# Performance work log

Hardware: AMD Instinct MI355X
Metric: run time of the kernel (lower is better)

The kernel has to match this reference:

```python
import jax, jax.numpy as jnp
import numpy as np

D_MODEL = 1024
H = 16
D_K = D_MODEL // H
B, S = 2, 2048

def setup_inputs() -> dict:
    key = jax.random.key(0)
    ks = jax.random.split(key, 13)
    scale = 1.0 / np.sqrt(D_MODEL)
    mk = lambda k: jax.random.normal(k, (D_MODEL, D_MODEL), dtype=jnp.float32) * scale
    return {
        'q': jax.random.normal(ks[0], (B, S, D_MODEL), dtype=jnp.float32),
        'k': jax.random.normal(ks[1], (B, S, D_MODEL), dtype=jnp.float32),
        'v': jax.random.normal(ks[2], (B, S, D_MODEL), dtype=jnp.float32),
        'mask': jax.random.randint(ks[3], (B, 1, S, S), 0, 2, dtype=jnp.int32),
        'wq': mk(ks[4]), 'bq': jnp.zeros((D_MODEL,), jnp.float32),
        'wk': mk(ks[5]), 'bk': jnp.zeros((D_MODEL,), jnp.float32),
        'wv': mk(ks[6]), 'bv': jnp.zeros((D_MODEL,), jnp.float32),
        'wo': mk(ks[7]), 'bo': jnp.zeros((D_MODEL,), jnp.float32),
    }

def reference(q, k, v, mask, wq, bq, wk, bk, wv, bv, wo, bo):
    b, s, _ = q.shape
    # linear projections then split heads: [B,S,D] -> [B,H,S,Dk]
    def proj(x, w, bias):
        y = x @ w + bias
        return y.reshape(b, -1, H, D_K).transpose(0, 2, 1, 3)
    Q = proj(q, wq, bq)
    K = proj(k, wk, bk)
    V = proj(v, wv, bv)
    scores = jnp.einsum('bhqd,bhkd->bhqk', Q, K) / jnp.sqrt(jnp.float32(D_K))
    # faithful to source: masked positions are set to 1e-9 (not -inf)
    scores = jnp.where(mask == 0, jnp.float32(1e-9), scores)
    attn = jax.nn.softmax(scores, axis=-1)  # dropout is identity in eval mode
    x = jnp.einsum('bhqk,bhkd->bhqd', attn, V)
    x = x.transpose(0, 2, 1, 3).reshape(b, s, D_MODEL)
    return x @ wo + bo
```

## Files before the change

### kernel.cpp

```cpp
#include <hip/hip_runtime.h>
#include <hip/hip_bf16.h>

#define DM 1024
#define HEADS 16
#define DKK 64
#define BB 2
#define SS 2048
#define MROWS (BB*SS)

typedef __attribute__((ext_vector_type(8))) short bf16x8;
typedef __attribute__((ext_vector_type(4))) float f32x4;
typedef __attribute__((ext_vector_type(2))) unsigned int uv2;
typedef __hip_bfloat16 bf16;

#define SC2 0.1803368801f
#define MB2 1.442695041e-9f

__device__ __forceinline__ void async16(const void* g, void* l) {
    __builtin_amdgcn_global_load_lds((const __attribute__((address_space(1))) void*)g,
                                     (__attribute__((address_space(3))) void*)l, 16, 0, 0);
}

__global__ void prep_kernel(const float* __restrict__ q, const float* __restrict__ k,
                            const float* __restrict__ v,
                            const float* __restrict__ wq, const float* __restrict__ wk,
                            const float* __restrict__ wv, const float* __restrict__ wo,
                            const int* __restrict__ mask,
                            bf16* __restrict__ qkv, bf16* __restrict__ wcat,
                            unsigned long long* __restrict__ bits) {
    __shared__ float tile[32][33];
    const int bid = blockIdx.x;
    const int tid = threadIdx.x;
    if (bid < 12288) {
        const int z = bid >> 12;
        const int i = ((bid & 4095) << 8) + tid;
        const float* src = z == 0 ? q : (z == 1 ? k : v);
        float4 val = ((const float4*)src)[i];
        union { bf16 b[4]; ushort4 u; } cvt;
        cvt.b[0] = __float2bfloat16(val.x);
        cvt.b[1] = __float2bfloat16(val.y);
        cvt.b[2] = __float2bfloat16(val.z);
        cvt.b[3] = __float2bfloat16(val.w);
        ((ushort4*)(qkv + (size_t)z * MROWS * DM))[i] = cvt.u;
    } else if (bid < 12288 + 4096) {
        const int t = bid - 12288;
        const int z = t >> 10;
        const int bx = t & 31, by = (t >> 5) & 31;
        const float* src = z == 0 ? wq : (z == 1 ? wk : (z == 2 ? wv : wo));
        bf16* dst = wcat + ((size_t)z << 20);
        const int tx = tid & 31, ty = tid >> 5;
        const int x = bx * 32 + tx, y0 = by * 32 + ty;
#pragma unroll
        for (int i = 0; i < 32; i += 8)
            tile[ty + i][tx] = src[(size_t)(y0 + i) * DM + x];
        __syncthreads();
        const int nx = by * 32 + tx, ny0 = bx * 32 + ty;
#pragma unroll
        for (int i = 0; i < 32; i += 8)
            dst[(size_t)(ny0 + i) * DM + nx] = __float2bfloat16(tile[tx][ty + i]);
    } else {
        const int i4 = ((bid - 16384) << 8) + tid;
        const int4 m = ((const int4*)mask)[i4];
        unsigned long long vv = (unsigned long long)(
            (m.x != 0 ? 1u : 0u) | (m.y != 0 ? 2u : 0u) |
            (m.z != 0 ? 4u : 0u) | (m.w != 0 ? 8u : 0u));
        vv <<= ((tid & 15) * 4);
        vv |= __shfl_xor(vv, 1);
        vv |= __shfl_xor(vv, 2);
        vv |= __shfl_xor(vv, 4);
        vv |= __shfl_xor(vv, 8);
        if ((tid & 15) == 0) bits[i4 >> 4] = vv;
    }
}

__global__ __launch_bounds__(256) void gemm_qkv(const bf16* __restrict__ qb, const bf16* __restrict__ kb,
                                                const bf16* __restrict__ vb, const bf16* __restrict__ wcat,
                                                const float* __restrict__ bq, const float* __restrict__ bk,
                                                const float* __restrict__ bv,
                                                bf16* __restrict__ Qh, bf16* __restrict__ Kh,
                                                bf16* __restrict__ Vt) {
    __shared__ __align__(16) bf16 lA[128 * 32];
    __shared__ __align__(16) bf16 lB[128 * 32];
    const int seg = blockIdx.x >> 3;
    const bf16* A    = seg == 0 ? qb : (seg == 1 ? kb : vb);
    const bf16* Bt   = wcat + ((size_t)seg << 20);
    const float* bias = seg == 0 ? bq : (seg == 1 ? bk : bv);

    const int tid  = threadIdx.x;
    const int lane = tid & 63;
    const int lm   = lane & 15;
    const int quad = lane >> 4;
    const int w    = tid >> 6;
    const int wm   = w >> 1, wn = w & 1;
    const int m0   = blockIdx.y * 128;
    const int n0   = (blockIdx.x & 7) * 128;
    const int wbase = w << 6;

    f32x4 acc[4][4];
#pragma unroll
    for (int i = 0; i < 4; ++i)
#pragma unroll
        for (int j = 0; j < 4; ++j) acc[i][j] = (f32x4){0.f, 0.f, 0.f, 0.f};

    for (int kt = 0; kt < DM / 32; ++kt) {
#pragma unroll
        for (int r = 0; r < 2; ++r) {
            const int idx = r * 256 + tid;
            const int row = idx >> 2;
            const int kc  = idx & 3;
            async16(A + (size_t)(m0 + row) * DM + kt * 32 + kc * 8,
                    (char*)lA + (size_t)(r * 256 + wbase) * 16);
            async16(Bt + (size_t)(n0 + row) * DM + kt * 32 + kc * 8,
                    (char*)lB + (size_t)(r * 256 + wbase) * 16);
        }
        __syncthreads();
        bf16x8 af[4], bb[4];
#pragma unroll
        for (int mt = 0; mt < 4; ++mt)
            af[mt] = *(const bf16x8*)&lA[(wm * 64 + mt * 16 + lm) * 32 + quad * 8];
#pragma unroll
        for (int nt = 0; nt < 4; ++nt)
            bb[nt] = *(const bf16x8*)&lB[(wn * 64 + nt * 16 + lm) * 32 + quad * 8];
#pragma unroll
        for (int mt = 0; mt < 4; ++mt)
#pragma unroll
            for (int nt = 0; nt < 4; ++nt)
                acc[mt][nt] = __builtin_amdgcn_mfma_f32_16x16x32_bf16(af[mt], bb[nt], acc[mt][nt], 0, 0, 0);
        __syncthreads();
    }

    if (seg < 2) {
        bf16* outQK = seg == 0 ? Qh : Kh;
        const float oscale = (seg == 1) ? SC2 : 1.0f;
#pragma unroll
        for (int mt = 0; mt < 4; ++mt) {
#pragma unroll
            for (int nt = 0; nt < 4; ++nt) {
                const int gcol = n0 + wn * 64 + nt * 16 + lm;
                const float bvv = bias[gcol];
                const int h = gcol >> 6, d = gcol & 63;
#pragma unroll
                for (int r = 0; r < 4; ++r) {
                    const int grow = m0 + wm * 64 + mt * 16 + quad * 4 + r;
                    const int b = grow >> 11, s = grow & 2047;
                    const float val = (acc[mt][nt][r] + bvv) * oscale;
                    outQK[((size_t)(b * HEADS + h) * SS + s) * DKK + d] = __float2bfloat16(val);
                }
            }
        }
    } else {
#pragma unroll
        for (int mt = 0; mt < 4; ++mt) {
#pragma unroll
            for (int nt = 0; nt < 4; ++nt) {
                const int gcol = n0 + wn * 64 + nt * 16 + lm;
                const float bvv = bias[gcol];
                const int h = gcol >> 6, d = gcol & 63;
                const int growb = m0 + wm * 64 + mt * 16 + quad * 4;
                const int b = growb >> 11, s = growb & 2047;
                union { bf16 hh[4]; uint2 u; } pk;
#pragma unroll
                for (int r = 0; r < 4; ++r) pk.hh[r] = __float2bfloat16(acc[mt][nt][r] + bvv);
                *(uint2*)&Vt[((size_t)(b * HEADS + h) * DKK + d) * SS + s] = pk.u;
            }
        }
    }
}

__global__ __launch_bounds__(256) void gemm_out(const bf16* __restrict__ A, const bf16* __restrict__ Bt,
                                                const float* __restrict__ bias, float* __restrict__ outp) {
    __shared__ __align__(16) bf16 lA[128 * 32];
    __shared__ __align__(16) bf16 lB[64 * 32];
    const int tid  = threadIdx.x;
    const int lane = tid & 63;
    const int lm   = lane & 15;
    const int quad = lane >> 4;
    const int w    = tid >> 6;
    const int m0   = blockIdx.y * 128;
    const int n0   = blockIdx.x * 64;
    const int wbase = w << 6;

    f32x4 acc[2][4];
#pragma unroll
    for (int i = 0; i < 2; ++i)
#pragma unroll
        for (int j = 0; j < 4; ++j) acc[i][j] = (f32x4){0.f, 0.f, 0.f, 0.f};

    for (int kt = 0; kt < DM / 32; ++kt) {
#pragma unroll
        for (int r = 0; r < 2; ++r) {
            const int idx = r * 256 + tid;
            const int row = idx >> 2;
            const int kc  = idx & 3;
            async16(A + (size_t)(m0 + row) * DM + kt * 32 + kc * 8,
                    (char*)lA + (size_t)(r * 256 + wbase) * 16);
        }
        {
            const int row = tid >> 2;
            const int kc  = tid & 3;
            async16(Bt + (size_t)(n0 + row) * DM + kt * 32 + kc * 8,
                    (char*)lB + (size_t)(wbase) * 16);
        }
        __syncthreads();
        bf16x8 af[2], bb[4];
#pragma unroll
        for (int mt = 0; mt < 2; ++mt)
            af[mt] = *(const bf16x8*)&lA[(w * 32 + mt * 16 + lm) * 32 + quad * 8];
#pragma unroll
        for (int nt = 0; nt < 4; ++nt)
            bb[nt] = *(const bf16x8*)&lB[(nt * 16 + lm) * 32 + quad * 8];
#pragma unroll
        for (int mt = 0; mt < 2; ++mt)
#pragma unroll
            for (int nt = 0; nt < 4; ++nt)
                acc[mt][nt] = __builtin_amdgcn_mfma_f32_16x16x32_bf16(af[mt], bb[nt], acc[mt][nt], 0, 0, 0);
        __syncthreads();
    }

#pragma unroll
    for (int mt = 0; mt < 2; ++mt)
#pragma unroll
        for (int nt = 0; nt < 4; ++nt) {
            const int gcol = n0 + nt * 16 + lm;
            const float bvv = bias[gcol];
#pragma unroll
            for (int r = 0; r < 4; ++r) {
                const int grow = m0 + w * 32 + mt * 16 + quad * 4 + r;
                outp[(size_t)grow * DM + gcol] = acc[mt][nt][r] + bvv;
            }
        }
}

__global__ __launch_bounds__(512, 8) void attn_kernel(const bf16* __restrict__ Qh, const bf16* __restrict__ Kh,
                                                      const bf16* __restrict__ Vt,
                                                      const unsigned long long* __restrict__ mbits,
                                                      bf16* __restrict__ ctx) {
    __shared__ __align__(16) bf16 ldsK[2][64 * 64];
    __shared__ __align__(16) bf16 ldsV[2][64 * 64];

    const int tid  = threadIdx.x;
    const int lane = tid & 63;
    const int lm   = lane & 15;
    const int quad = lane >> 4;
    const int w    = tid >> 6;
    const int wq   = w & 3;
    const int kh   = w >> 2;
    const int bh   = blockIdx.y;
    const int b    = bh >> 4;
    const int h    = bh & 15;
    const int q0   = blockIdx.x * 64;
    const int qrow = q0 + wq * 16 + lm;

    const int x0 = quad ^ (lm & 7);
    const int x1 = x0 ^ 4;
    const int xh = kh ? x1 : x0;

    const int srow = tid >> 3;
    const int sw   = (tid & 7) ^ (srow & 7);
    const bf16* pK = Kh + (size_t)bh * SS * DKK + (size_t)srow * DKK + sw * 8;
    const bf16* pV = Vt + (size_t)bh * DKK * SS + (size_t)srow * SS + sw * 8;
    char* dK[2] = { (char*)ldsK[0] + (size_t)(w * 64) * 16, (char*)ldsK[1] + (size_t)(w * 64) * 16 };
    char* dV[2] = { (char*)ldsV[0] + (size_t)(w * 64) * 16, (char*)ldsV[1] + (size_t)(w * 64) * 16 };

    const bf16* qp = Qh + ((size_t)bh * SS + qrow) * DKK;
    const bf16x8 aq0 = *(const bf16x8*)(qp + quad * 8);
    const bf16x8 aq1 = *(const bf16x8*)(qp + 32 + quad * 8);

    const unsigned long long* pm = mbits + ((size_t)b * SS + qrow) * (SS / 64);

    f32x4 o[4];
#pragma unroll
    for (int i = 0; i < 4; ++i) o[i] = (f32x4){0.f, 0.f, 0.f, 0.f};
    float lsum = 0.f;

    async16(pK, dK[0]);
    async16(pV, dV[0]);
    __syncthreads();

    const int nkt = SS / 64;
    const int mshift = kh * 32 + quad * 4;

    auto body = [&](int it, int cur) {
        const unsigned long long mw = pm[it];
        if (it + 1 < nkt) {
            const int nb = cur ^ 1;
            async16(pK + (size_t)(it + 1) * 64 * DKK, dK[nb]);
            async16(pV + (size_t)(it + 1) * 64, dV[nb]);
        }
        const bf16* lk = ldsK[cur];
        const bf16* lv = ldsV[cur];

        f32x4 sc[2];
#pragma unroll
        for (int mtl = 0; mtl < 2; ++mtl) {
            const int mt = kh * 2 + mtl;
            sc[mtl] = (f32x4){0.f, 0.f, 0.f, 0.f};
            const bf16x8 kf0 = *(const bf16x8*)&lk[(mt * 16 + lm) * 64 + x0 * 8];
            const bf16x8 kf1 = *(const bf16x8*)&lk[(mt * 16 + lm) * 64 + x1 * 8];
            sc[mtl] = __builtin_amdgcn_mfma_f32_16x16x32_bf16(kf0, aq0, sc[mtl], 0, 0, 0);
            sc[mtl] = __builtin_amdgcn_mfma_f32_16x16x32_bf16(kf1, aq1, sc[mtl], 0, 0, 0);
        }

        const unsigned long long mq = mw >> mshift;
        unsigned wds[4];
#pragma unroll
        for (int mtl = 0; mtl < 2; ++mtl) {
            const unsigned mmt = (unsigned)(mq >> (mtl * 16));
#pragma unroll
            for (int pp = 0; pp < 2; ++pp) {
                union { bf16 hh[2]; unsigned u; } wu;
#pragma unroll
                for (int j = 0; j < 2; ++j) {
                    const int r = pp * 2 + j;
                    const float sv = ((mmt >> r) & 1u) ? sc[mtl][r] : MB2;
                    const float p = __builtin_amdgcn_exp2f(sv);
                    lsum += p;
                    wu.hh[j] = __float2bfloat16(p);
                }
                wds[mtl * 2 + pp] = wu.u;
            }
        }

        const uv2 s1 = __builtin_amdgcn_permlane32_swap(wds[0], wds[2], false, false);
        const uv2 s2 = __builtin_amdgcn_permlane16_swap(s1.x, s1.y, false, false);
        const uv2 s3 = __builtin_amdgcn_permlane32_swap(wds[1], wds[3], false, false);
        const uv2 s4 = __builtin_amdgcn_permlane16_swap(s3.x, s3.y, false, false);
        union { unsigned u[4]; bf16x8 v; } pf;
        pf.u[0] = s2.x; pf.u[1] = s4.x; pf.u[2] = s2.y; pf.u[3] = s4.y;

#pragma unroll
        for (int mt = 0; mt < 4; ++mt) {
            const bf16x8 vf = *(const bf16x8*)&lv[(mt * 16 + lm) * 64 + xh * 8];
            o[mt] = __builtin_amdgcn_mfma_f32_16x16x32_bf16(vf, pf.v, o[mt], 0, 0, 0);
        }
        __syncthreads();
    };

    for (int it = 0; it < nkt; it += 2) {
        body(it, 0);
        body(it + 1, 1);
    }

    lsum += __shfl_xor(lsum, 16);
    lsum += __shfl_xor(lsum, 32);

    float* oshare = (float*)ldsK;
    float* lshare = (float*)ldsV;
    if (kh == 1) {
#pragma unroll
        for (int mt = 0; mt < 4; ++mt)
            *(f32x4*)&oshare[(size_t)(wq * 16 + lm) * 64 + mt * 16 + quad * 4] = o[mt];
        if (lane < 16) lshare[wq * 16 + lane] = lsum;
    }
    __syncthreads();
    if (kh == 0) {
#pragma unroll
        for (int mt = 0; mt < 4; ++mt)
            o[mt] += *(const f32x4*)&oshare[(size_t)(wq * 16 + lm) * 64 + mt * 16 + quad * 4];
        lsum += lshare[wq * 16 + lm];
        const float rl = 1.0f / lsum;

        bf16* crow = ctx + ((size_t)b * SS + qrow) * DM + h * DKK;
#pragma unroll
        for (int mt = 0; mt < 4; ++mt) {
            union { bf16 hh[4]; uint2 u; } pk;
#pragma unroll
            for (int r = 0; r < 4; ++r) pk.hh[r] = __float2bfloat16(o[mt][r] * rl);
            *(uint2*)&crow[mt * 16 + quad * 4] = pk.u;
        }
    }
}

extern "C" void kernel_launch(void* const* d_in, const int* in_sizes, int n_in,
                              void* d_out, int out_size, void* d_ws, size_t ws_size,
                              hipStream_t stream) {
    const float* q  = (const float*)d_in[0];
    const float* k  = (const float*)d_in[1];
    const float* v  = (const float*)d_in[2];
    const int* mask = (const int*)d_in[3];
    const float* wq = (const float*)d_in[4];
    const float* bq = (const float*)d_in[5];
    const float* wk = (const float*)d_in[6];
    const float* bk = (const float*)d_in[7];
    const float* wv = (const float*)d_in[8];
    const float* bv = (const float*)d_in[9];
    const float* wo = (const float*)d_in[10];
    const float* bo = (const float*)d_in[11];

    const size_t MB = 1ull << 20;
    char* ws = (char*)d_ws;
    bf16* qkv  = (bf16*)(ws + 0 * MB);
    bf16* wcat = (bf16*)(ws + 24 * MB);
    bf16* wot  = (bf16*)(ws + 30 * MB);
    bf16* Qh   = (bf16*)(ws + 32 * MB);
    bf16* Kh   = (bf16*)(ws + 40 * MB);
    bf16* Vt   = (bf16*)(ws + 48 * MB);
    bf16* ctx  = (bf16*)(ws + 56 * MB);
    unsigned long long* mbits = (unsigned long long*)(ws + 64 * MB);

    prep_kernel<<<24576, 256, 0, stream>>>(q, k, v, wq, wk, wv, wo, mask, qkv, wcat, mbits);

    gemm_qkv<<<dim3(24, 32), 256, 0, stream>>>(qkv, qkv + (size_t)MROWS * DM, qkv + 2 * (size_t)MROWS * DM,
                                               wcat, bq, bk, bv, Qh, Kh, Vt);

    attn_kernel<<<dim3(SS / 64, BB * HEADS), 512, 0, stream>>>(Qh, Kh, Vt, mbits, ctx);

    gemm_out<<<dim3(DM / 64, MROWS / 128), 256, 0, stream>>>(ctx, wot, bo, (float*)d_out);
}
```

Before: 282.8 us.

## Process 128 query rows per attention block to reuse K/V tiles

Each wave now handles two 16-row query tiles instead of one, so every block covers 128 queries. K and V tiles loaded into LDS are reused for twice as many MFMAs, which halves global K/V traffic and the number of LDS loads per unit of work. The grid is halved and launch bounds lowered to 4 blocks per CU to allow more registers. The reduction scratch uses padded rows (stride 66) in one merged shared buffer. The cost is roughly twice the accumulator and score registers and fewer blocks for latency hiding.

```diff
diff --git a/kernel.cpp b/kernel.cpp
--- a/kernel.cpp
+++ b/kernel.cpp
@@ -231,25 +231,28 @@
         }
 }
 
-__global__ __launch_bounds__(512, 8) void attn_kernel(const bf16* __restrict__ Qh, const bf16* __restrict__ Kh,
+__global__ __launch_bounds__(512, 4) void attn_kernel(const bf16* __restrict__ Qh, const bf16* __restrict__ Kh,
                                                       const bf16* __restrict__ Vt,
                                                       const unsigned long long* __restrict__ mbits,
                                                       bf16* __restrict__ ctx) {
-    __shared__ __align__(16) bf16 ldsK[2][64 * 64];
-    __shared__ __align__(16) bf16 ldsV[2][64 * 64];
+    __shared__ __align__(16) char smem[34816];
+    bf16* ldsKb = (bf16*)smem;
+    bf16* ldsVb = (bf16*)(smem + 16384);
+    float* oshare = (float*)smem;
+    float* lshare = (float*)(smem + 33792);
 
     const int tid  = threadIdx.x;
     const int lane = tid & 63;
     const int lm   = lane & 15;
     const int quad = lane >> 4;
     const int w    = tid >> 6;
-    const int wq   = w & 3;
+    const int qg   = w & 3;
     const int kh   = w >> 2;
     const int bh   = blockIdx.y;
     const int b    = bh >> 4;
     const int h    = bh & 15;
-    const int q0   = blockIdx.x * 64;
-    const int qrow = q0 + wq * 16 + lm;
+    const int q0   = blockIdx.x * 128;
+    const int qrow0 = q0 + qg * 32 + lm;
 
     const int x0 = quad ^ (lm & 7);
     const int x1 = x0 ^ 4;
@@ -259,19 +262,25 @@
     const int sw   = (tid & 7) ^ (srow & 7);
     const bf16* pK = Kh + (size_t)bh * SS * DKK + (size_t)srow * DKK + sw * 8;
     const bf16* pV = Vt + (size_t)bh * DKK * SS + (size_t)srow * SS + sw * 8;
-    char* dK[2] = { (char*)ldsK[0] + (size_t)(w * 64) * 16, (char*)ldsK[1] + (size_t)(w * 64) * 16 };
-    char* dV[2] = { (char*)ldsV[0] + (size_t)(w * 64) * 16, (char*)ldsV[1] + (size_t)(w * 64) * 16 };
-
-    const bf16* qp = Qh + ((size_t)bh * SS + qrow) * DKK;
-    const bf16x8 aq0 = *(const bf16x8*)(qp + quad * 8);
-    const bf16x8 aq1 = *(const bf16x8*)(qp + 32 + quad * 8);
-
-    const unsigned long long* pm = mbits + ((size_t)b * SS + qrow) * (SS / 64);
-
-    f32x4 o[4];
-#pragma unroll
-    for (int i = 0; i < 4; ++i) o[i] = (f32x4){0.f, 0.f, 0.f, 0.f};
-    float lsum = 0.f;
+    char* dK[2] = { (char*)smem + (size_t)tid * 16, (char*)smem + 8192 + (size_t)tid * 16 };
+    char* dV[2] = { (char*)smem + 16384 + (size_t)tid * 16, (char*)smem + 24576 + (size_t)tid * 16 };
+
+    const bf16* qp0 = Qh + ((size_t)bh * SS + qrow0) * DKK;
+    bf16x8 aq[2][2];
+    aq[0][0] = *(const bf16x8*)(qp0 + quad * 8);
+    aq[0][1] = *(const bf16x8*)(qp0 + 32 + quad * 8);
+    aq[1][0] = *(const bf16x8*)(qp0 + 16 * DKK + quad * 8);
+    aq[1][1] = *(const bf16x8*)(qp0 + 16 * DKK + 32 + quad * 8);
+
+    const unsigned long long* pm0 = mbits + ((size_t)b * SS + qrow0) * (SS / 64);
+    const unsigned long long* pm1 = pm0 + 16 * (SS / 64);
+
+    f32x4 o[2][4];
+#pragma unroll
+    for (int i = 0; i < 2; ++i)
+#pragma unroll
+        for (int j = 0; j < 4; ++j) o[i][j] = (f32x4){0.f, 0.f, 0.f, 0.f};
+    float lsum[2] = {0.f, 0.f};
 
     async16(pK, dK[0]);
     async16(pV, dV[0]);
@@ -281,57 +290,66 @@
     const int mshift = kh * 32 + quad * 4;
 
     auto body = [&](int it, int cur) {
-        const unsigned long long mw = pm[it];
+        const unsigned long long mw0 = pm0[it];
+        const unsigned long long mw1 = pm1[it];
         if (it + 1 < nkt) {
             const int nb = cur ^ 1;
             async16(pK + (size_t)(it + 1) * 64 * DKK, dK[nb]);
             async16(pV + (size_t)(it + 1) * 64, dV[nb]);
         }
-        const bf16* lk = ldsK[cur];
-        const bf16* lv = ldsV[cur];
-
-        f32x4 sc[2];
+        const bf16* lk = ldsKb + cur * 4096;
+        const bf16* lv = ldsVb + cur * 4096;
+
+        f32x4 sc[2][2];
 #pragma unroll
         for (int mtl = 0; mtl < 2; ++mtl) {
             const int mt = kh * 2 + mtl;
-            sc[mtl] = (f32x4){0.f, 0.f, 0.f, 0.f};
             const bf16x8 kf0 = *(const bf16x8*)&lk[(mt * 16 + lm) * 64 + x0 * 8];
             const bf16x8 kf1 = *(const bf16x8*)&lk[(mt * 16 + lm) * 64 + x1 * 8];
-            sc[mtl] = __builtin_amdgcn_mfma_f32_16x16x32_bf16(kf0, aq0, sc[mtl], 0, 0, 0);
-            sc[mtl] = __builtin_amdgcn_mfma_f32_16x16x32_bf16(kf1, aq1, sc[mtl], 0, 0, 0);
-        }
-
-        const unsigned long long mq = mw >> mshift;
-        unsigned wds[4];
-#pragma unroll
-        for (int mtl = 0; mtl < 2; ++mtl) {
-            const unsigned mmt = (unsigned)(mq >> (mtl * 16));
-#pragma unroll
-            for (int pp = 0; pp < 2; ++pp) {
-                union { bf16 hh[2]; unsigned u; } wu;
-#pragma unroll
-                for (int j = 0; j < 2; ++j) {
-                    const int r = pp * 2 + j;
-                    const float sv = ((mmt >> r) & 1u) ? sc[mtl][r] : MB2;
-                    const float p = __builtin_amdgcn_exp2f(sv);
-                    lsum += p;
-                    wu.hh[j] = __float2bfloat16(p);
+#pragma unroll
+            for (int qb = 0; qb < 2; ++qb) {
+                sc[qb][mtl] = (f32x4){0.f, 0.f, 0.f, 0.f};
+                sc[qb][mtl] = __builtin_amdgcn_mfma_f32_16x16x32_bf16(kf0, aq[qb][0], sc[qb][mtl], 0, 0, 0);
+                sc[qb][mtl] = __builtin_amdgcn_mfma_f32_16x16x32_bf16(kf1, aq[qb][1], sc[qb][mtl], 0, 0, 0);
+            }
+        }
+
+        bf16x8 pf[2];
+#pragma unroll
+        for (int qb = 0; qb < 2; ++qb) {
+            const unsigned long long mq = (qb ? mw1 : mw0) >> mshift;
+            unsigned wds[4];
+#pragma unroll
+            for (int mtl = 0; mtl < 2; ++mtl) {
+                const unsigned mmt = (unsigned)(mq >> (mtl * 16));
+#pragma unroll
+                for (int pp = 0; pp < 2; ++pp) {
+                    union { bf16 hh[2]; unsigned u; } wu;
+#pragma unroll
+                    for (int j = 0; j < 2; ++j) {
+                        const int r = pp * 2 + j;
+                        const float sv = ((mmt >> r) & 1u) ? sc[qb][mtl][r] : MB2;
+                        const float p = __builtin_amdgcn_exp2f(sv);
+                        lsum[qb] += p;
+                        wu.hh[j] = __float2bfloat16(p);
+                    }
+                    wds[mtl * 2 + pp] = wu.u;
                 }
-                wds[mtl * 2 + pp] = wu.u;
-            }
-        }
-
-        const uv2 s1 = __builtin_amdgcn_permlane32_swap(wds[0], wds[2], false, false);
-        const uv2 s2 = __builtin_amdgcn_permlane16_swap(s1.x, s1.y, false, false);
-        const uv2 s3 = __builtin_amdgcn_permlane32_swap(wds[1], wds[3], false, false);
-        const uv2 s4 = __builtin_amdgcn_permlane16_swap(s3.x, s3.y, false, false);
-        union { unsigned u[4]; bf16x8 v; } pf;
-        pf.u[0] = s2.x; pf.u[1] = s4.x; pf.u[2] = s2.y; pf.u[3] = s4.y;
+            }
+            const uv2 s1 = __builtin_amdgcn_permlane32_swap(wds[0], wds[2], false, false);
+            const uv2 s2 = __builtin_amdgcn_permlane16_swap(s1.x, s1.y, false, false);
+            const uv2 s3 = __builtin_amdgcn_permlane32_swap(wds[1], wds[3], false, false);
+            const uv2 s4 = __builtin_amdgcn_permlane16_swap(s3.x, s3.y, false, false);
+            union { unsigned u[4]; bf16x8 v; } pfu;
+            pfu.u[0] = s2.x; pfu.u[1] = s4.x; pfu.u[2] = s2.y; pfu.u[3] = s4.y;
+            pf[qb] = pfu.v;
+        }
 
 #pragma unroll
         for (int mt = 0; mt < 4; ++mt) {
             const bf16x8 vf = *(const bf16x8*)&lv[(mt * 16 + lm) * 64 + xh * 8];
-            o[mt] = __builtin_amdgcn_mfma_f32_16x16x32_bf16(vf, pf.v, o[mt], 0, 0, 0);
+            o[0][mt] = __builtin_amdgcn_mfma_f32_16x16x32_bf16(vf, pf[0], o[0][mt], 0, 0, 0);
+            o[1][mt] = __builtin_amdgcn_mfma_f32_16x16x32_bf16(vf, pf[1], o[1][mt], 0, 0, 0);
         }
         __syncthreads();
     };
@@ -341,32 +359,37 @@
         body(it + 1, 1);
     }
 
-    lsum += __shfl_xor(lsum, 16);
-    lsum += __shfl_xor(lsum, 32);
-
-    float* oshare = (float*)ldsK;
-    float* lshare = (float*)ldsV;
+#pragma unroll
+    for (int qb = 0; qb < 2; ++qb) {
+        lsum[qb] += __shfl_xor(lsum[qb], 16);
+        lsum[qb] += __shfl_xor(lsum[qb], 32);
+    }
+
     if (kh == 1) {
 #pragma unroll
-        for (int mt = 0; mt < 4; ++mt)
-            *(f32x4*)&oshare[(size_t)(wq * 16 + lm) * 64 + mt * 16 + quad * 4] = o[mt];
-        if (lane < 16) lshare[wq * 16 + lane] = lsum;
+        for (int qb = 0; qb < 2; ++qb)
+#pragma unroll
+            for (int mt = 0; mt < 4; ++mt)
+                *(f32x4*)&oshare[(size_t)(qg * 32 + qb * 16 + lm) * 66 + mt * 16 + quad * 4] = o[qb][mt];
+        if (lane < 32) lshare[qg * 32 + lane] = lsum[lane >> 4];
     }
     __syncthreads();
     if (kh == 0) {
 #pragma unroll
-        for (int mt = 0; mt < 4; ++mt)
-            o[mt] += *(const f32x4*)&oshare[(size_t)(wq * 16 + lm) * 64 + mt * 16 + quad * 4];
-        lsum += lshare[wq * 16 + lm];
-        const float rl = 1.0f / lsum;
-
-        bf16* crow = ctx + ((size_t)b * SS + qrow) * DM + h * DKK;
-#pragma unroll
-        for (int mt = 0; mt < 4; ++mt) {
-            union { bf16 hh[4]; uint2 u; } pk;
-#pragma unroll
-            for (int r = 0; r < 4; ++r) pk.hh[r] = __float2bfloat16(o[mt][r] * rl);
-            *(uint2*)&crow[mt * 16 + quad * 4] = pk.u;
+        for (int qb = 0; qb < 2; ++qb) {
+#pragma unroll
+            for (int mt = 0; mt < 4; ++mt)
+                o[qb][mt] += *(const f32x4*)&oshare[(size_t)(qg * 32 + qb * 16 + lm) * 66 + mt * 16 + quad * 4];
+            const float l = lsum[qb] + lshare[qg * 32 + qb * 16 + lm];
+            const float rl = 1.0f / l;
+            bf16* crow = ctx + ((size_t)b * SS + qrow0 + qb * 16) * DM + h * DKK;
+#pragma unroll
+            for (int mt = 0; mt < 4; ++mt) {
+                union { bf16 hh[4]; uint2 u; } pk;
+#pragma unroll
+                for (int r = 0; r < 4; ++r) pk.hh[r] = __float2bfloat16(o[qb][mt][r] * rl);
+                *(uint2*)&crow[mt * 16 + quad * 4] = pk.u;
+            }
         }
     }
 }
@@ -403,7 +426,7 @@
     gemm_qkv<<<dim3(24, 32), 256, 0, stream>>>(qkv, qkv + (size_t)MROWS * DM, qkv + 2 * (size_t)MROWS * DM,
                                                wcat, bq, bk, bv, Qh, Kh, Vt);
 
-    attn_kernel<<<dim3(SS / 64, BB * HEADS), 512, 0, stream>>>(Qh, Kh, Vt, mbits, ctx);
+    attn_kernel<<<dim3(SS / 128, BB * HEADS), 512, 0, stream>>>(Qh, Kh, Vt, mbits, ctx);
 
     gemm_out<<<dim3(DM / 64, MROWS / 128), 256, 0, stream>>>(ctx, wot, bo, (float*)d_out);
 }
```

Measured after the change: 277.3 us. About the same (-1.9%).
